# Optimization experiments

Hardware: AMD Instinct MI355X
Metric: run time of the kernel (lower is better)

## Reference

```python
import jax, jax.numpy as jnp
import numpy as np

N = 50000      # nodes
E = 800000     # edges (before self loops)
F_IN = 64      # num_features
HID = 64       # hidden_channels
NCLS = 10      # num_classes
NG = 512       # number of graphs in batch
NEG_SLOPE = 0.2


def setup_inputs() -> dict:
    key = jax.random.key(0)
    ks = jax.random.split(key, 14)
    def g(k, shape, scale=0.1):
        return jax.random.normal(k, shape, dtype=jnp.float32) * scale
    inp = {
        "x": jax.random.normal(ks[0], (N, F_IN), dtype=jnp.float32),
        "edge_index": jax.random.randint(ks[1], (2, E), 0, N, dtype=jnp.int64),
        "batch": jnp.sort(jax.random.randint(ks[2], (N,), 0, NG, dtype=jnp.int64)),
        # conv1: GATv2Conv(F_IN, HID, heads=2), separate lin_l / lin_r, att [H, C]
        "Wl1": g(ks[3], (F_IN, 2 * HID)),
        "Wr1": g(ks[4], (F_IN, 2 * HID)),
        "att1": g(ks[5], (2, HID)),
        "b1": g(ks[6], (2 * HID,)),
        # conv2: GATv2Conv(2*HID, HID, heads=1)
        "Wl2": g(ks[7], (2 * HID, HID)),
        "Wr2": g(ks[8], (2 * HID, HID)),
        "att2": g(ks[9], (1, HID)),
        "b2": g(ks[10], (HID,)),
        # final classifier
        "lin_w": g(ks[11], (HID, NCLS)),
        "lin_b": g(ks[12], (NCLS,)),
    }
    return inp


def _gatv2(x, Wl, Wr, att, b, src, dst, n, heads, outc):
    """GATv2Conv: e = a^T LeakyReLU(Wl x_j + Wr x_i), segment-softmax over dst."""
    xl = (x @ Wl).reshape(n, heads, outc)   # source transform
    xr = (x @ Wr).reshape(n, heads, outc)   # target transform
    e = jax.nn.leaky_relu(xl[src] + xr[dst], NEG_SLOPE)      # [E, H, C]
    logits = jnp.einsum('ehc,hc->eh', e, att)                # [E, H]
    m = jax.lax.stop_gradient(jax.ops.segment_max(logits, dst, num_segments=n))
    ex = jnp.exp(logits - m[dst])
    denom = jax.ops.segment_sum(ex, dst, num_segments=n)     # [N, H]
    alpha = ex / denom[dst]                                  # [E, H]
    out = jax.ops.segment_sum(alpha[:, :, None] * xl[src], dst, num_segments=n)
    return out.reshape(n, heads * outc) + b


def reference(x, edge_index, batch, Wl1, Wr1, att1, b1, Wl2, Wr2, att2, b2, lin_w, lin_b):
    n = x.shape[0]
    loop = jnp.arange(n, dtype=edge_index.dtype)
    src = jnp.concatenate([edge_index[0], loop])   # add_self_loops=True
    dst = jnp.concatenate([edge_index[1], loop])
    h = jax.nn.elu(_gatv2(x, Wl1, Wr1, att1, b1, src, dst, n, 2, HID))   # [N, 2*HID]
    h = _gatv2(h, Wl2, Wr2, att2, b2, src, dst, n, 1, HID)               # [N, HID]
    # global mean pool over graph ids
    sums = jax.ops.segment_sum(h, batch, num_segments=NG)                # [NG, HID]
    cnt = jax.ops.segment_sum(jnp.ones((n,), h.dtype), batch, num_segments=NG)
    pooled = sums / jnp.maximum(cnt, 1.0)[:, None]
    # dropout is identity in eval mode
    return pooled @ lin_w + lin_b                                        # [NG, NCLS]
```

## Files before the change

kernel.cpp:

```cpp
#include <hip/hip_runtime.h>
#include <hip/hip_bf16.h>

#define F_IN 64
#define HID 64
#define NCLS 10
#define NG 512

__device__ __forceinline__ unsigned short f2bf(float f) {
    unsigned int u = __float_as_uint(f);
    unsigned int r = (u + 0x7fffu + ((u >> 16) & 1u)) >> 16;
    return (unsigned short)r;
}
__device__ __forceinline__ float bf2f(unsigned short h) {
    return __uint_as_float(((unsigned int)h) << 16);
}

__global__ void count_gbound_kernel(const int* __restrict__ ei, int* __restrict__ deg,
                                    const int* __restrict__ batch, int* __restrict__ gstart,
                                    int E_, int N_, int cblk) {
    int b = blockIdx.x;
    if (b < cblk) {
        int e = b * 256 + threadIdx.x;
        if (e < E_) atomicAdd(&deg[ei[E_ + e]], 1);
    } else {
        int i = (b - cblk) * 256 + threadIdx.x;
        if (i >= N_) return;
        int bi = batch[i];
        int bprev = (i == 0) ? -1 : batch[i - 1];
        for (int g = bprev + 1; g <= bi; ++g) gstart[g] = i;
        if (i == N_ - 1)
            for (int g = bi + 1; g <= NG; ++g) gstart[g] = N_;
    }
}

__global__ void scan_local_kernel(const int* __restrict__ deg, int* __restrict__ rs_part,
                                  int* __restrict__ blksum, int N_) {
    __shared__ int tmp[256];
    int t = threadIdx.x;
    int i = blockIdx.x * 256 + t;
    int v = (i < N_) ? deg[i] : 0;
    tmp[t] = v;
    __syncthreads();
    for (int off = 1; off < 256; off <<= 1) {
        int add = (t >= off) ? tmp[t - off] : 0;
        __syncthreads();
        tmp[t] += add;
        __syncthreads();
    }
    if (i < N_) rs_part[i] = tmp[t] - v;
    if (t == 255) blksum[blockIdx.x] = tmp[255];
}

__global__ void scan_final_kernel(const int* __restrict__ rs_part,
                                  const int* __restrict__ blksum,
                                  int* __restrict__ rs, int* __restrict__ cursor,
                                  int N_, int E_, int nblk) {
    __shared__ int tmp[256];
    int t = threadIdx.x;
    int b = blockIdx.x;
    tmp[t] = (t < b && t < nblk) ? blksum[t] : 0;
    __syncthreads();
    for (int off = 128; off > 0; off >>= 1) {
        if (t < off) tmp[t] += tmp[t + off];
        __syncthreads();
    }
    int off0 = tmp[0];
    int i = b * 256 + t;
    if (i < N_) {
        int v = rs_part[i] + off0;
        rs[i] = v;
        cursor[i] = v;
    }
    if (i == 0) rs[N_] = E_;
}

__global__ void scatter_kernel(const int* __restrict__ ei, int* __restrict__ cursor,
                               int* __restrict__ csr_src, int E_) {
    int e = blockIdx.x * 256 + threadIdx.x;
    if (e < E_) {
        int d = ei[E_ + e];
        int pos = atomicAdd(&cursor[d], 1);
        csr_src[pos] = ei[e];
    }
}

__global__ void gemm1_kernel(const float* __restrict__ x,
                             const float* __restrict__ Wl,
                             const float* __restrict__ Wr,
                             unsigned short* __restrict__ xlb,
                             float* __restrict__ xr,
                             int N_) {
    __shared__ float xs[8 * 64];
    int r0 = blockIdx.x * 8;
    int t = threadIdx.x;
    for (int i = t; i < 8 * 64; i += 256) {
        int r = i >> 6;
        xs[i] = (r0 + r < N_) ? x[(long)(r0 + r) * 64 + (i & 63)] : 0.f;
    }
    __syncthreads();
    const float* W = (t < 128) ? Wl : Wr;
    int col = t & 127;
    float acc[8] = {0.f, 0.f, 0.f, 0.f, 0.f, 0.f, 0.f, 0.f};
    for (int k = 0; k < 64; ++k) {
        float w = W[k * 128 + col];
#pragma unroll
        for (int r = 0; r < 8; ++r) acc[r] += xs[r * 64 + k] * w;
    }
    if (t < 128) {
#pragma unroll
        for (int r = 0; r < 8; ++r)
            if (r0 + r < N_) xlb[(long)(r0 + r) * 128 + col] = f2bf(acc[r]);
    } else {
#pragma unroll
        for (int r = 0; r < 8; ++r)
            if (r0 + r < N_) xr[(long)(r0 + r) * 128 + col] = acc[r];
    }
}

__global__ void gemm2_kernel(const float* __restrict__ h1,
                             const float* __restrict__ Wl,
                             const float* __restrict__ Wr,
                             unsigned short* __restrict__ xlb,
                             float* __restrict__ xr,
                             int N_) {
    __shared__ float hs[8 * 128];
    int r0 = blockIdx.x * 8;
    int t = threadIdx.x;
    for (int i = t; i < 8 * 128; i += 128) {
        int r = i >> 7;
        hs[i] = (r0 + r < N_) ? h1[(long)(r0 + r) * 128 + (i & 127)] : 0.f;
    }
    __syncthreads();
    const float* W = (t < 64) ? Wl : Wr;
    int col = t & 63;
    float acc[8] = {0.f, 0.f, 0.f, 0.f, 0.f, 0.f, 0.f, 0.f};
    for (int k = 0; k < 128; ++k) {
        float w = W[k * 64 + col];
#pragma unroll
        for (int r = 0; r < 8; ++r) acc[r] += hs[r * 128 + k] * w;
    }
    if (t < 64) {
#pragma unroll
        for (int r = 0; r < 8; ++r)
            if (r0 + r < N_) xlb[(long)(r0 + r) * 64 + col] = f2bf(acc[r]);
    } else {
#pragma unroll
        for (int r = 0; r < 8; ++r)
            if (r0 + r < N_) xr[(long)(r0 + r) * 64 + col] = acc[r];
    }
}

__global__ void gat1_kernel(const unsigned short* __restrict__ xlb,
                            float* __restrict__ xr,
                            const float* __restrict__ att,
                            const float* __restrict__ b1,
                            const int* __restrict__ rs,
                            const int* __restrict__ csr_src,
                            int N_) {
    int d = (int)(((long)blockIdx.x * blockDim.x + threadIdx.x) >> 6);
    int lane = threadIdx.x & 63;
    if (d >= N_) return;
    int slot = lane >> 5;
    int c8 = lane & 31;
    long rowoff = (long)d * 128 + c8 * 4;
    const float4 xr4 = *(const float4*)(xr + rowoff);
    const float4 at4 = *(const float4*)(att + c8 * 4);

    int k0 = rs[d], k1 = rs[d + 1];
    int cnt = k1 - k0 + 1;

    float4 acc = make_float4(0.f, 0.f, 0.f, 0.f);
    float den = 0.f;
    for (int c0 = 0; c0 < cnt; c0 += 64) {
        int wl = c0 + lane;
        int myidx = (wl >= 1 && wl < cnt) ? csr_src[k0 + wl - 1] : d;
        int lim = min(64, cnt - c0);
        for (int p = 0; p < lim; p += 4) {
            int e0 = p + slot, e1 = p + 2 + slot;
            int s0 = __shfl(myidx, e0, 64);
            int s1 = __shfl(myidx, e1, 64);
            bool v0 = e0 < lim, v1 = e1 < lim;
            ushort4 u0 = *(const ushort4*)(xlb + (long)s0 * 128 + c8 * 4);
            ushort4 u1 = *(const ushort4*)(xlb + (long)s1 * 128 + c8 * 4);
            float4 a0 = make_float4(bf2f(u0.x), bf2f(u0.y), bf2f(u0.z), bf2f(u0.w));
            float4 a1 = make_float4(bf2f(u1.x), bf2f(u1.y), bf2f(u1.z), bf2f(u1.w));
            float t, p0, p1;
            t = a0.x + xr4.x; t = fmaxf(t, 0.2f * t); p0  = at4.x * t;
            t = a0.y + xr4.y; t = fmaxf(t, 0.2f * t); p0 += at4.y * t;
            t = a0.z + xr4.z; t = fmaxf(t, 0.2f * t); p0 += at4.z * t;
            t = a0.w + xr4.w; t = fmaxf(t, 0.2f * t); p0 += at4.w * t;
            t = a1.x + xr4.x; t = fmaxf(t, 0.2f * t); p1  = at4.x * t;
            t = a1.y + xr4.y; t = fmaxf(t, 0.2f * t); p1 += at4.y * t;
            t = a1.z + xr4.z; t = fmaxf(t, 0.2f * t); p1 += at4.z * t;
            t = a1.w + xr4.w; t = fmaxf(t, 0.2f * t); p1 += at4.w * t;
            p0 += __shfl_xor(p0, 1, 64);  p1 += __shfl_xor(p1, 1, 64);
            p0 += __shfl_xor(p0, 2, 64);  p1 += __shfl_xor(p1, 2, 64);
            p0 += __shfl_xor(p0, 4, 64);  p1 += __shfl_xor(p1, 4, 64);
            p0 += __shfl_xor(p0, 8, 64);  p1 += __shfl_xor(p1, 8, 64);
            float w0 = v0 ? __expf(p0) : 0.f;
            float w1 = v1 ? __expf(p1) : 0.f;
            acc.x += w0 * a0.x + w1 * a1.x;
            acc.y += w0 * a0.y + w1 * a1.y;
            acc.z += w0 * a0.z + w1 * a1.z;
            acc.w += w0 * a0.w + w1 * a1.w;
            den += w0 + w1;
        }
    }
    acc.x += __shfl_xor(acc.x, 32, 64);
    acc.y += __shfl_xor(acc.y, 32, 64);
    acc.z += __shfl_xor(acc.z, 32, 64);
    acc.w += __shfl_xor(acc.w, 32, 64);
    den   += __shfl_xor(den, 32, 64);
    if (slot == 0) {
        const float4 b4 = *(const float4*)(b1 + c8 * 4);
        float inv = 1.f / den;
        float4 v;
        v.x = acc.x * inv + b4.x; v.x = (v.x > 0.f) ? v.x : __expf(v.x) - 1.f;
        v.y = acc.y * inv + b4.y; v.y = (v.y > 0.f) ? v.y : __expf(v.y) - 1.f;
        v.z = acc.z * inv + b4.z; v.z = (v.z > 0.f) ? v.z : __expf(v.z) - 1.f;
        v.w = acc.w * inv + b4.w; v.w = (v.w > 0.f) ? v.w : __expf(v.w) - 1.f;
        *(float4*)(xr + rowoff) = v;
    }
}

__global__ void gat2_kernel(const unsigned short* __restrict__ xlb,
                            const float* __restrict__ xr,
                            const float* __restrict__ att,
                            const float* __restrict__ b2,
                            const int* __restrict__ rs,
                            const int* __restrict__ csr_src,
                            float* __restrict__ h2,
                            int N_) {
    int d = (int)(((long)blockIdx.x * blockDim.x + threadIdx.x) >> 6);
    int lane = threadIdx.x & 63;
    if (d >= N_) return;
    int g = lane >> 4;
    int c4 = lane & 15;
    long rowoff = (long)d * 64 + c4 * 4;
    const float4 xr4 = *(const float4*)(xr + rowoff);
    const float4 at4 = *(const float4*)(att + c4 * 4);

    int k0 = rs[d], k1 = rs[d + 1];
    int cnt = k1 - k0 + 1;

    float4 acc = make_float4(0.f, 0.f, 0.f, 0.f);
    float den = 0.f;
    for (int c0 = 0; c0 < cnt; c0 += 64) {
        int wl = c0 + lane;
        int myidx = (wl >= 1 && wl < cnt) ? csr_src[k0 + wl - 1] : d;
        int lim = min(64, cnt - c0);
        for (int p = 0; p < lim; p += 8) {
            int e0 = p + g, e1 = p + 4 + g;
            int s0 = __shfl(myidx, e0, 64);
            int s1 = __shfl(myidx, e1, 64);
            bool v0 = e0 < lim, v1 = e1 < lim;
            ushort4 u0 = *(const ushort4*)(xlb + (long)s0 * 64 + c4 * 4);
            ushort4 u1 = *(const ushort4*)(xlb + (long)s1 * 64 + c4 * 4);
            float4 a0 = make_float4(bf2f(u0.x), bf2f(u0.y), bf2f(u0.z), bf2f(u0.w));
            float4 a1 = make_float4(bf2f(u1.x), bf2f(u1.y), bf2f(u1.z), bf2f(u1.w));
            float t, p0, p1;
            t = a0.x + xr4.x; t = fmaxf(t, 0.2f * t); p0  = at4.x * t;
            t = a0.y + xr4.y; t = fmaxf(t, 0.2f * t); p0 += at4.y * t;
            t = a0.z + xr4.z; t = fmaxf(t, 0.2f * t); p0 += at4.z * t;
            t = a0.w + xr4.w; t = fmaxf(t, 0.2f * t); p0 += at4.w * t;
            t = a1.x + xr4.x; t = fmaxf(t, 0.2f * t); p1  = at4.x * t;
            t = a1.y + xr4.y; t = fmaxf(t, 0.2f * t); p1 += at4.y * t;
            t = a1.z + xr4.z; t = fmaxf(t, 0.2f * t); p1 += at4.z * t;
            t = a1.w + xr4.w; t = fmaxf(t, 0.2f * t); p1 += at4.w * t;
            p0 += __shfl_xor(p0, 1, 64);  p1 += __shfl_xor(p1, 1, 64);
            p0 += __shfl_xor(p0, 2, 64);  p1 += __shfl_xor(p1, 2, 64);
            p0 += __shfl_xor(p0, 4, 64);  p1 += __shfl_xor(p1, 4, 64);
            p0 += __shfl_xor(p0, 8, 64);  p1 += __shfl_xor(p1, 8, 64);
            float w0 = v0 ? __expf(p0) : 0.f;
            float w1 = v1 ? __expf(p1) : 0.f;
            acc.x += w0 * a0.x + w1 * a1.x;
            acc.y += w0 * a0.y + w1 * a1.y;
            acc.z += w0 * a0.z + w1 * a1.z;
            acc.w += w0 * a0.w + w1 * a1.w;
            den += w0 + w1;
        }
    }
#pragma unroll
    for (int m = 16; m < 64; m <<= 1) {
        acc.x += __shfl_xor(acc.x, m, 64);
        acc.y += __shfl_xor(acc.y, m, 64);
        acc.z += __shfl_xor(acc.z, m, 64);
        acc.w += __shfl_xor(acc.w, m, 64);
        den   += __shfl_xor(den, m, 64);
    }
    if (g == 0) {
        const float4 b4 = *(const float4*)(b2 + c4 * 4);
        float inv = 1.f / den;
        float4 v;
        v.x = acc.x * inv + b4.x;
        v.y = acc.y * inv + b4.y;
        v.z = acc.z * inv + b4.z;
        v.w = acc.w * inv + b4.w;
        *(float4*)(h2 + rowoff) = v;
    }
}

__global__ void pool_final_kernel(const float* __restrict__ h2,
                                  const int* __restrict__ gstart,
                                  const float* __restrict__ lin_w,
                                  const float* __restrict__ lin_b,
                                  float* __restrict__ out) {
    int g = blockIdx.x;
    int lane = threadIdx.x;
    int s = gstart[g], e = gstart[g + 1];
    float acc = 0.f;
    int i = s;
    for (; i + 3 < e; i += 4) {
        float v0 = h2[(long)i * 64 + lane];
        float v1 = h2[(long)(i + 1) * 64 + lane];
        float v2 = h2[(long)(i + 2) * 64 + lane];
        float v3 = h2[(long)(i + 3) * 64 + lane];
        acc += (v0 + v1) + (v2 + v3);
    }
    for (; i < e; ++i) acc += h2[(long)i * 64 + lane];
    float pc = acc / fmaxf((float)(e - s), 1.f);
    __shared__ float pl[64];
    pl[lane] = pc;
    __syncthreads();
    if (lane < NCLS) {
        float o = lin_b[lane];
#pragma unroll 8
        for (int c = 0; c < 64; ++c) o += pl[c] * lin_w[c * NCLS + lane];
        out[g * NCLS + lane] = o;
    }
}

extern "C" void kernel_launch(void* const* d_in, const int* in_sizes, int n_in,
                              void* d_out, int out_size, void* d_ws, size_t ws_size,
                              hipStream_t stream) {
    const float* x     = (const float*)d_in[0];
    const int*   ei    = (const int*)d_in[1];
    const int*   batch = (const int*)d_in[2];
    const float* Wl1   = (const float*)d_in[3];
    const float* Wr1   = (const float*)d_in[4];
    const float* att1  = (const float*)d_in[5];
    const float* b1    = (const float*)d_in[6];
    const float* Wl2   = (const float*)d_in[7];
    const float* Wr2   = (const float*)d_in[8];
    const float* att2  = (const float*)d_in[9];
    const float* b2    = (const float*)d_in[10];
    const float* lin_w = (const float*)d_in[11];
    const float* lin_b = (const float*)d_in[12];
    float* out = (float*)d_out;

    const int N_ = in_sizes[0] / F_IN;
    const int E_ = in_sizes[1] / 2;

    float* ws = (float*)d_ws;
    float* B = ws;
    unsigned short* xl1b = (unsigned short*)(B + (long)N_ * 128);
    unsigned short* xl2b = xl1b + (long)N_ * 128;
    float* xr2 = (float*)(xl2b + (long)N_ * 64);
    int* deg     = (int*)(xr2 + (long)N_ * 64);
    int* rs      = deg + N_;
    int* cursor  = rs + N_ + 1;
    int* csr_src = cursor + N_;
    int* gstart  = csr_src + E_;
    int* rs_part = gstart + NG + 1;
    int* blksum  = rs_part + N_;
    float* h2 = B;

    const int nblk = (N_ + 255) / 256;
    const int cblk = (E_ + 255) / 256;

    hipMemsetAsync(deg, 0, (size_t)N_ * sizeof(int), stream);
    count_gbound_kernel<<<cblk + nblk, 256, 0, stream>>>(ei, deg, batch, gstart,
                                                         E_, N_, cblk);
    scan_local_kernel<<<nblk, 256, 0, stream>>>(deg, rs_part, blksum, N_);
    scan_final_kernel<<<nblk, 256, 0, stream>>>(rs_part, blksum, rs, cursor, N_, E_, nblk);
    scatter_kernel<<<cblk, 256, 0, stream>>>(ei, cursor, csr_src, E_);
    gemm1_kernel<<<(N_ + 7) / 8, 256, 0, stream>>>(x, Wl1, Wr1, xl1b, B, N_);
    {
        int blocks = (int)(((long)N_ * 64 + 255) / 256);
        gat1_kernel<<<blocks, 256, 0, stream>>>(xl1b, B, att1, b1, rs, csr_src, N_);
    }
    gemm2_kernel<<<(N_ + 7) / 8, 128, 0, stream>>>(B, Wl2, Wr2, xl2b, xr2, N_);
    {
        int blocks = (int)(((long)N_ * 64 + 255) / 256);
        gat2_kernel<<<blocks, 256, 0, stream>>>(xl2b, xr2, att2, b2, rs, csr_src, h2, N_);
    }
    pool_final_kernel<<<NG, 64, 0, stream>>>(h2, gstart, lin_w, lin_b, out);
}
```

Before: 272.0 us.

## Shard degree count and CSR scatter atomics by destination range across XCD-interleaved blocks

The degree-count and scatter kernels now split destination nodes into 8 slices, assigning block index mod 8 to a slice. Each block grid-strides over the edge list and only performs atomics for destinations in its slice. The intent is to keep atomics on a given region of deg/cursor within one XCD's L2, assuming round-robin block-to-XCD placement, and so avoid cross-die atomic traffic. The cost is that every edge's destination index is read 8 times, and the result depends on how the hardware places blocks.

Result: faster. 253.9 us (-6.6%).

```diff
diff --git a/kernel.cpp b/kernel.cpp
--- a/kernel.cpp
+++ b/kernel.cpp
@@ -17,13 +17,20 @@
 
 __global__ void count_gbound_kernel(const int* __restrict__ ei, int* __restrict__ deg,
                                     const int* __restrict__ batch, int* __restrict__ gstart,
-                                    int E_, int N_, int cblk) {
+                                    int E_, int N_, int csh) {
     int b = blockIdx.x;
-    if (b < cblk) {
-        int e = b * 256 + threadIdx.x;
-        if (e < E_) atomicAdd(&deg[ei[E_ + e]], 1);
+    if (b < csh * 8) {
+        int shard = b & 7;
+        int chunk = b >> 3;
+        int slice = (N_ + 7) >> 3;
+        int lo = shard * slice, hi = min(N_, lo + slice);
+        int stride = csh * 256;
+        for (int e = chunk * 256 + threadIdx.x; e < E_; e += stride) {
+            int d = ei[E_ + e];
+            if (d >= lo && d < hi) atomicAdd(&deg[d], 1);
+        }
     } else {
-        int i = (b - cblk) * 256 + threadIdx.x;
+        int i = (b - csh * 8) * 256 + threadIdx.x;
         if (i >= N_) return;
         int bi = batch[i];
         int bprev = (i == 0) ? -1 : batch[i - 1];
@@ -75,12 +82,18 @@
 }
 
 __global__ void scatter_kernel(const int* __restrict__ ei, int* __restrict__ cursor,
-                               int* __restrict__ csr_src, int E_) {
-    int e = blockIdx.x * 256 + threadIdx.x;
-    if (e < E_) {
+                               int* __restrict__ csr_src, int E_, int N_, int csh) {
+    int shard = blockIdx.x & 7;
+    int chunk = blockIdx.x >> 3;
+    int slice = (N_ + 7) >> 3;
+    int lo = shard * slice, hi = min(N_, lo + slice);
+    int stride = csh * 256;
+    for (int e = chunk * 256 + threadIdx.x; e < E_; e += stride) {
         int d = ei[E_ + e];
-        int pos = atomicAdd(&cursor[d], 1);
-        csr_src[pos] = ei[e];
+        if (d >= lo && d < hi) {
+            int pos = atomicAdd(&cursor[d], 1);
+            csr_src[pos] = ei[e];
+        }
     }
 }
 
@@ -366,14 +379,14 @@
     float* h2 = B;
 
     const int nblk = (N_ + 255) / 256;
-    const int cblk = (E_ + 255) / 256;
+    const int csh  = 391;
 
     hipMemsetAsync(deg, 0, (size_t)N_ * sizeof(int), stream);
-    count_gbound_kernel<<<cblk + nblk, 256, 0, stream>>>(ei, deg, batch, gstart,
-                                                         E_, N_, cblk);
+    count_gbound_kernel<<<csh * 8 + nblk, 256, 0, stream>>>(ei, deg, batch, gstart,
+                                                            E_, N_, csh);
     scan_local_kernel<<<nblk, 256, 0, stream>>>(deg, rs_part, blksum, N_);
     scan_final_kernel<<<nblk, 256, 0, stream>>>(rs_part, blksum, rs, cursor, N_, E_, nblk);
-    scatter_kernel<<<cblk, 256, 0, stream>>>(ei, cursor, csr_src, E_);
+    scatter_kernel<<<csh * 8, 256, 0, stream>>>(ei, cursor, csr_src, E_, N_, csh);
     gemm1_kernel<<<(N_ + 7) / 8, 256, 0, stream>>>(x, Wl1, Wr1, xl1b, B, N_);
     {
         int blocks = (int)(((long)N_ * 64 + 255) / 256);
```
